# Optimization experiments

Hardware: AMD Instinct MI355X
Metric: run time of the kernel (lower is better)

## Reference

```python
import jax, jax.numpy as jnp
import numpy as np

D_MODEL = 512
N_HEADS = 8
D_HEAD = D_MODEL // N_HEADS
EPS = 1e-6


def setup_inputs() -> dict:
    key = jax.random.key(0)
    ks = jax.random.split(key, 9)
    B, S = 2, 2048
    scale = 0.02
    x = jax.random.normal(ks[0], (B, S, D_MODEL), dtype=jnp.float32)
    Wq = jax.random.normal(ks[1], (D_MODEL, D_MODEL), dtype=jnp.float32) * scale
    Wk = jax.random.normal(ks[2], (D_MODEL, D_MODEL), dtype=jnp.float32) * scale
    Wv = jax.random.normal(ks[3], (D_MODEL, D_MODEL), dtype=jnp.float32) * scale
    Wo = jax.random.normal(ks[4], (D_MODEL, D_MODEL), dtype=jnp.float32) * scale
    bq = jax.random.normal(ks[5], (D_MODEL,), dtype=jnp.float32) * scale
    bk = jax.random.normal(ks[6], (D_MODEL,), dtype=jnp.float32) * scale
    bv = jax.random.normal(ks[7], (D_MODEL,), dtype=jnp.float32) * scale
    bo = jax.random.normal(ks[8], (D_MODEL,), dtype=jnp.float32) * scale
    return {"x": x, "Wq": Wq, "bq": bq, "Wk": Wk, "bk": bk,
            "Wv": Wv, "bv": bv, "Wo": Wo, "bo": bo}


def _split_heads(t, B, S):
    # [B,S,D] -> [B,H,S,dh]
    return t.reshape(B, S, N_HEADS, D_HEAD).transpose(0, 2, 1, 3)


def reference(x, Wq, bq, Wk, bk, Wv, bv, Wo, bo):
    B, S, _ = x.shape
    q = _split_heads(x @ Wq.T + bq, B, S)
    k = _split_heads(x @ Wk.T + bk, B, S)
    v = _split_heads(x @ Wv.T + bv, B, S)
    # 'relu' kernel applied to Q and K
    q = jax.nn.relu(q)
    k = jax.nn.relu(k)
    # K_sum: [B,H,S,1] -- per-position sum over head dim; note it broadcasts
    # over the KEY axis of attn, i.e. each QUERY row n is divided by K_sum[n]
    k_sum = k.sum(axis=-1, keepdims=True)
    attn = jnp.einsum('bhnd,bhmd->bhnm', q, k) / (k_sum + EPS)
    attn = jax.nn.softmax(attn, axis=-1)
    out = jnp.einsum('bhnm,bhmd->bhnd', attn, v)
    out = out.transpose(0, 2, 1, 3).reshape(B, S, D_MODEL)
    return (out @ Wo.T + bo, attn)
```

## Files before the change

### kernel.cpp

```cpp
#include <hip/hip_runtime.h>
#include <stdint.h>


typedef __attribute__((ext_vector_type(8))) short short8;
typedef __attribute__((ext_vector_type(4))) float f4;

#define MFMA(a, b, c) __builtin_amdgcn_mfma_f32_16x16x32_bf16(a, b, c, 0, 0, 0)

struct __align__(8) us4 { uint16_t a, b, c, d; };

__device__ __forceinline__ uint16_t f2bf(float f) {
  union { float f; uint32_t u; } v; v.f = f;
  uint32_t u = v.u;
  return (uint16_t)((u + 0x7fffu + ((u >> 16) & 1u)) >> 16);
}
__device__ __forceinline__ float bf2f(uint16_t u) {
  union { uint32_t u; float f; } v; v.u = ((uint32_t)u) << 16; return v.f;
}
__device__ __forceinline__ us4 pack4(float4 v) {
  us4 r; r.a = f2bf(v.x); r.b = f2bf(v.y); r.c = f2bf(v.z); r.d = f2bf(v.w); return r;
}

__device__ __forceinline__ void async16(const uint16_t* g, uint16_t* l) {
  __builtin_amdgcn_global_load_lds(
      (const __attribute__((address_space(1))) void*)g,
      (__attribute__((address_space(3))) void*)l, 16, 0, 0);
}

__global__ __launch_bounds__(256) void convert_kernel(
    const float* __restrict__ x, const float* __restrict__ Wq,
    const float* __restrict__ Wk, const float* __restrict__ Wv,
    const float* __restrict__ Wo, uint16_t* __restrict__ xb,
    uint16_t* __restrict__ W3, uint16_t* __restrict__ Wob) {
  int i = blockIdx.x * 256 + threadIdx.x;
  ((us4*)xb)[i] = pack4(((const float4*)x)[i]);
  if (i < 65536) {
    ((us4*)W3)[i]          = pack4(((const float4*)Wq)[i]);
    ((us4*)W3)[65536 + i]  = pack4(((const float4*)Wk)[i]);
    ((us4*)W3)[131072 + i] = pack4(((const float4*)Wv)[i]);
    ((us4*)Wob)[i]         = pack4(((const float4*)Wo)[i]);
  }
}

__device__ __forceinline__ void gemm_loop(
    const uint16_t* __restrict__ A, const uint16_t* __restrict__ Bt,
    int row0, int col0, uint16_t* Alds, uint16_t* Blds, f4 (&acc)[4][4]) {
  const int tid = threadIdx.x;
  const int w = tid >> 6, lane = tid & 63;
  const int c = lane & 15, quad = lane >> 4;
  const int wm = w >> 1, wn = w & 1;
  const int srow = lane >> 2;
  const int sslot = ((lane & 3) ^ ((lane >> 2) & 3) ^ ((lane >> 4) & 3)) * 8;
  const uint16_t* Asrc = A + (size_t)(row0 + srow) * 512 + sslot;
  const uint16_t* Bsrc = Bt + (size_t)(col0 + srow) * 512 + sslot;
  const int posv = (quad ^ (c & 3) ^ (c >> 2)) * 8;
  for (int k0 = 0; k0 < 512; k0 += 32) {
    __syncthreads();
#pragma unroll
    for (int chh = 0; chh < 2; ++chh) {
      int ch = w * 2 + chh;
      async16(Asrc + (size_t)ch * 16 * 512 + k0, Alds + ch * 512);
      async16(Bsrc + (size_t)ch * 16 * 512 + k0, Blds + ch * 512);
    }
    __syncthreads();
    short8 af[4], bf[4];
#pragma unroll
    for (int mi = 0; mi < 4; ++mi)
      af[mi] = *(const short8*)&Alds[(wm * 64 + mi * 16 + c) * 32 + posv];
#pragma unroll
    for (int ni = 0; ni < 4; ++ni)
      bf[ni] = *(const short8*)&Blds[(wn * 64 + ni * 16 + c) * 32 + posv];
#pragma unroll
    for (int mi = 0; mi < 4; ++mi)
#pragma unroll
      for (int ni = 0; ni < 4; ++ni)
        acc[mi][ni] = MFMA(af[mi], bf[ni], acc[mi][ni]);
  }
}

__global__ __launch_bounds__(256) void qkv_gemm(
    const uint16_t* __restrict__ xb, const uint16_t* __restrict__ W3,
    const float* __restrict__ bq, const float* __restrict__ bk,
    const float* __restrict__ bv, uint16_t* __restrict__ Qb,
    uint16_t* __restrict__ Kb, uint16_t* __restrict__ Vt) {
  __shared__ __align__(16) uint16_t Alds[128 * 32];
  __shared__ __align__(16) uint16_t Blds[128 * 32];
  __shared__ __align__(16) uint16_t Ct[128 * 136];
  f4 acc[4][4] = {};
  const int row0 = blockIdx.y * 128, col0 = blockIdx.x * 128;
  gemm_loop(xb, W3, row0, col0, Alds, Blds, acc);
  const int tid = threadIdx.x, w = tid >> 6, lane = tid & 63;
  const int c = lane & 15, quad = lane >> 4;
  const int wm = w >> 1, wn = w & 1;
  const int r3 = col0 >> 9;
  if (r3 < 2) {
    const float* bias = (r3 == 0) ? bq : bk;
    uint16_t* dst = (r3 == 0) ? Qb : Kb;
#pragma unroll
    for (int mi = 0; mi < 4; ++mi)
#pragma unroll
      for (int ni = 0; ni < 4; ++ni)
#pragma unroll
        for (int r = 0; r < 4; ++r) {
          int row = row0 + wm * 64 + mi * 16 + quad * 4 + r;
          int col = col0 + wn * 64 + ni * 16 + c;
          int o = col & 511;
          float v = acc[mi][ni][r] + bias[o];
          dst[(size_t)row * 512 + o] = f2bf(fmaxf(v, 0.0f));
        }
  } else {
#pragma unroll
    for (int mi = 0; mi < 4; ++mi)
#pragma unroll
      for (int ni = 0; ni < 4; ++ni)
#pragma unroll
        for (int r = 0; r < 4; ++r) {
          int sl = wm * 64 + mi * 16 + quad * 4 + r;
          int cl = wn * 64 + ni * 16 + c;
          int o = (col0 + cl) & 511;
          Ct[sl * 136 + cl] = f2bf(acc[mi][ni][r] + bv[o]);
        }
    __syncthreads();
    const int b = row0 >> 11, s0 = row0 & 2047;
    const int cl = tid >> 1, half = tid & 1;
    const int ocol = (col0 - 1024) + cl;
    uint16_t* vdst = Vt + (size_t)(b * 512 + ocol) * 2048 + s0 + half * 64;
#pragma unroll
    for (int g = 0; g < 8; ++g) {
      union { short8 v; uint16_t e[8]; } o8;
#pragma unroll
      for (int jj = 0; jj < 8; ++jj)
        o8.e[jj] = Ct[(half * 64 + g * 8 + jj) * 136 + cl];
      *(short8*)(vdst + g * 8) = o8.v;
    }
  }
}

__global__ __launch_bounds__(256) void proj_gemm(
    const uint16_t* __restrict__ Ob, const uint16_t* __restrict__ Wob,
    const float* __restrict__ bo, float* __restrict__ out) {
  __shared__ __align__(16) uint16_t Alds[128 * 32];
  __shared__ __align__(16) uint16_t Blds[128 * 32];
  f4 acc[4][4] = {};
  const int row0 = blockIdx.y * 128, col0 = blockIdx.x * 128;
  gemm_loop(Ob, Wob, row0, col0, Alds, Blds, acc);
  const int tid = threadIdx.x, w = tid >> 6, lane = tid & 63;
  const int c = lane & 15, quad = lane >> 4;
  const int wm = w >> 1, wn = w & 1;
#pragma unroll
  for (int mi = 0; mi < 4; ++mi)
#pragma unroll
    for (int ni = 0; ni < 4; ++ni)
#pragma unroll
      for (int r = 0; r < 4; ++r) {
        int row = row0 + wm * 64 + mi * 16 + quad * 4 + r;
        int col = col0 + wn * 64 + ni * 16 + c;
        out[(size_t)row * 512 + col] = acc[mi][ni][r] + bo[col];
      }
}

__global__ __launch_bounds__(256) void ksum_kernel(
    const uint16_t* __restrict__ Kb, float* __restrict__ rq) {
  int t = blockIdx.x * 256 + threadIdx.x;
  int row = t >> 2, part = t & 3;
  const uint4* p = (const uint4*)(Kb + (size_t)row * 64 + part * 16);
  float s = 0.f;
#pragma unroll
  for (int g = 0; g < 2; ++g) {
    union { uint4 u; uint16_t e[8]; } v; v.u = p[g];
#pragma unroll
    for (int j = 0; j < 8; ++j) s += bf2f(v.e[j]);
  }
  s += __shfl_xor(s, 1, 4);
  s += __shfl_xor(s, 2, 4);
  if (part == 0) rq[row] = 1.0f / (s + 1e-6f);
}

__global__ __launch_bounds__(256) void attn_kernel(
    const uint16_t* __restrict__ Qb, const uint16_t* __restrict__ Kb,
    const uint16_t* __restrict__ Vt, const float* __restrict__ rq,
    float* __restrict__ attn, uint16_t* __restrict__ Ob) {
  __shared__ __align__(16) uint16_t Klds[64 * 64];
  __shared__ __align__(16) uint16_t Vlds[64 * 64];
  __shared__ __align__(16) float Pw[4][16 * 64];
  const int tid = threadIdx.x, w = tid >> 6, lane = tid & 63;
  const int c = lane & 15, quad = lane >> 4, c7 = c & 7;
  const int bid = blockIdx.x;
  const int bh = (bid & 7) * 2 + ((bid >> 3) & 1);
  const int qt = bid >> 4;
  const int b = bh >> 3, h = bh & 7;
  const int n0 = qt * 64;
  const int rbase = b * 2048 + n0;
  const uint16_t* qptr = Qb + (size_t)(rbase + w * 16 + c) * 512 + h * 64 + quad * 8;
  short8 aq0 = *(const short8*)qptr;
  short8 aq1 = *(const short8*)(qptr + 32);
  float rqv[4];
#pragma unroll
  for (int r = 0; r < 4; ++r)
    rqv[r] = rq[(size_t)(rbase + w * 16 + quad * 4 + r) * 8 + h];
  const int vsrow = lane >> 3;
  const int vslot = ((lane & 7) ^ vsrow) * 8;
  const uint16_t* Ksrc = Kb + (size_t)(b * 2048) * 512 + h * 64 + vslot;
  const uint16_t* Vsrc = Vt + (size_t)(bh * 64) * 2048 + vslot;

  float lsum[4] = {0.f, 0.f, 0.f, 0.f};
  for (int kt = 0; kt < 32; ++kt) {
    __syncthreads();
#pragma unroll
    for (int chh = 0; chh < 2; ++chh) {
      int ch = w * 2 + chh;
      async16(Ksrc + (size_t)(kt * 64 + ch * 8 + vsrow) * 512, Klds + ch * 512);
    }
    __syncthreads();
#pragma unroll
    for (int ni = 0; ni < 4; ++ni) {
      const uint16_t* kp = &Klds[(ni * 16 + c) * 64];
      short8 bk0 = *(const short8*)(kp + ((quad ^ c7) * 8));
      short8 bk1 = *(const short8*)(kp + (((quad + 4) ^ c7) * 8));
      f4 s = {};
      s = MFMA(aq0, bk0, s);
      s = MFMA(aq1, bk1, s);
#pragma unroll
      for (int r = 0; r < 4; ++r) lsum[r] += __expf(s[r] * rqv[r]);
    }
  }
  float rli[4];
#pragma unroll
  for (int r = 0; r < 4; ++r) {
    float v = lsum[r];
    v += __shfl_xor(v, 1, 16);
    v += __shfl_xor(v, 2, 16);
    v += __shfl_xor(v, 4, 16);
    v += __shfl_xor(v, 8, 16);
    rli[r] = 1.0f / v;
  }

  f4 oacc[4] = {};
  float* arowc = attn + ((size_t)bh * 2048 + n0 + w * 16 + c) * 2048;
  float* Pme = Pw[w];
  for (int kt = 0; kt < 32; ++kt) {
    __syncthreads();
#pragma unroll
    for (int chh = 0; chh < 2; ++chh) {
      int ch = w * 2 + chh;
      async16(Ksrc + (size_t)(kt * 64 + ch * 8 + vsrow) * 512, Klds + ch * 512);
      async16(Vsrc + (size_t)(ch * 8 + vsrow) * 2048 + kt * 64, Vlds + ch * 512);
    }
    __syncthreads();
#pragma unroll
    for (int ni = 0; ni < 4; ++ni) {
      const uint16_t* kp = &Klds[(ni * 16 + c) * 64];
      short8 bk0 = *(const short8*)(kp + ((quad ^ c7) * 8));
      short8 bk1 = *(const short8*)(kp + (((quad + 4) ^ c7) * 8));
      f4 s = {};
      s = MFMA(aq0, bk0, s);
      s = MFMA(aq1, bk1, s);
#pragma unroll
      for (int r = 0; r < 4; ++r) {
        int rowp = quad * 4 + r;
        float p = __expf(s[r] * rqv[r]) * rli[r];
        Pme[rowp * 64 + (((ni * 4 + (c >> 2)) ^ rowp) * 4) + (c & 3)] = p;
      }
    }
    asm volatile("s_waitcnt lgkmcnt(0)" ::: "memory");
#pragma unroll
    for (int ks = 0; ks < 2; ++ks) {
      int ch0 = ks * 8 + quad * 2;
      f4 p0 = *(const f4*)&Pme[c * 64 + ((ch0 ^ c) * 4)];
      f4 p1 = *(const f4*)&Pme[c * 64 + (((ch0 + 1) ^ c) * 4)];
      *(f4*)&arowc[kt * 64 + ch0 * 4] = p0;
      *(f4*)&arowc[kt * 64 + ch0 * 4 + 4] = p1;
      union { short8 v; uint16_t e[8]; } ap;
#pragma unroll
      for (int i = 0; i < 4; ++i) { ap.e[i] = f2bf(p0[i]); ap.e[4 + i] = f2bf(p1[i]); }
#pragma unroll
      for (int nj = 0; nj < 4; ++nj) {
        short8 bvv = *(const short8*)&Vlds[(nj * 16 + c) * 64 +
                                           (((ks * 4 + quad) ^ c7) * 8)];
        oacc[nj] = MFMA(ap.v, bvv, oacc[nj]);
      }
    }
  }
#pragma unroll
  for (int nj = 0; nj < 4; ++nj)
#pragma unroll
    for (int r = 0; r < 4; ++r)
      Ob[(size_t)(rbase + w * 16 + quad * 4 + r) * 512 + h * 64 + nj * 16 + c] =
          f2bf(oacc[nj][r]);
}

extern "C" void kernel_launch(void* const* d_in, const int* in_sizes, int n_in,
                              void* d_out, int out_size, void* d_ws, size_t ws_size,
                              hipStream_t stream) {
  const float* x  = (const float*)d_in[0];
  const float* Wq = (const float*)d_in[1];
  const float* bq = (const float*)d_in[2];
  const float* Wk = (const float*)d_in[3];
  const float* bk = (const float*)d_in[4];
  const float* Wv = (const float*)d_in[5];
  const float* bv = (const float*)d_in[6];
  const float* Wo = (const float*)d_in[7];
  const float* bo = (const float*)d_in[8];

  float* out0 = (float*)d_out;
  float* attn = out0 + (size_t)2 * 2048 * 512;

  uint8_t* ws = (uint8_t*)d_ws;
  uint16_t* xb  = (uint16_t*)(ws);
  uint16_t* W3  = (uint16_t*)(ws + 0x400000);
  uint16_t* Wob = (uint16_t*)(ws + 0x580000);
  uint16_t* Qb  = (uint16_t*)(ws + 0x600000);
  uint16_t* Kb  = (uint16_t*)(ws + 0xA00000);
  uint16_t* Vt  = (uint16_t*)(ws + 0xE00000);
  uint16_t* Ob  = (uint16_t*)(ws + 0x1200000);
  float*    rq  = (float*)  (ws + 0x1600000);

  convert_kernel<<<2048, 256, 0, stream>>>(x, Wq, Wk, Wv, Wo, xb, W3, Wob);
  qkv_gemm<<<dim3(12, 32), 256, 0, stream>>>(xb, W3, bq, bk, bv, Qb, Kb, Vt);
  ksum_kernel<<<512, 256, 0, stream>>>(Kb, rq);
  attn_kernel<<<512, 256, 0, stream>>>(Qb, Kb, Vt, rq, attn, Ob);
  proj_gemm<<<dim3(4, 32), 256, 0, stream>>>(Ob, Wob, bo, out0);
}
```

Measured before the change: 382.8 us.

## Double-buffer LDS tiles in GEMM and attention loops to overlap loads

Adds ping-pong LDS buffers to the shared GEMM loop and to both attention passes. The next K/V or A/B tile is issued with async global-to-LDS loads before computing on the current tile, and each iteration needs only one barrier instead of two. The aim is to hide global-load latency behind MFMA and exp work. In exchange it uses more LDS, which can lower occupancy. It also relies on the one end-of-iteration barrier being enough to ensure the async loads have completed, since no explicit vmcnt wait is added.

Result: no change. 378.6 us (-1.1%).

```diff
diff --git a/kernel.cpp b/kernel.cpp
--- a/kernel.cpp
+++ b/kernel.cpp
@@ -44,7 +44,8 @@
 
 __device__ __forceinline__ void gemm_loop(
     const uint16_t* __restrict__ A, const uint16_t* __restrict__ Bt,
-    int row0, int col0, uint16_t* Alds, uint16_t* Blds, f4 (&acc)[4][4]) {
+    int row0, int col0, uint16_t* A0, uint16_t* B0,
+    uint16_t* A1, uint16_t* B1, f4 (&acc)[4][4]) {
   const int tid = threadIdx.x;
   const int w = tid >> 6, lane = tid & 63;
   const int c = lane & 15, quad = lane >> 4;
@@ -54,27 +55,39 @@
   const uint16_t* Asrc = A + (size_t)(row0 + srow) * 512 + sslot;
   const uint16_t* Bsrc = Bt + (size_t)(col0 + srow) * 512 + sslot;
   const int posv = (quad ^ (c & 3) ^ (c >> 2)) * 8;
+#pragma unroll
+  for (int chh = 0; chh < 2; ++chh) {
+    int ch = w * 2 + chh;
+    async16(Asrc + (size_t)ch * 16 * 512, A0 + ch * 512);
+    async16(Bsrc + (size_t)ch * 16 * 512, B0 + ch * 512);
+  }
+  __syncthreads();
   for (int k0 = 0; k0 < 512; k0 += 32) {
+    const uint16_t* Ac = (k0 & 32) ? A1 : A0;
+    const uint16_t* Bc = (k0 & 32) ? B1 : B0;
+    if (k0 + 32 < 512) {
+      uint16_t* An = (k0 & 32) ? A0 : A1;
+      uint16_t* Bn = (k0 & 32) ? B0 : B1;
+#pragma unroll
+      for (int chh = 0; chh < 2; ++chh) {
+        int ch = w * 2 + chh;
+        async16(Asrc + (size_t)ch * 16 * 512 + (k0 + 32), An + ch * 512);
+        async16(Bsrc + (size_t)ch * 16 * 512 + (k0 + 32), Bn + ch * 512);
+      }
+    }
+    short8 af[4], bfr[4];
+#pragma unroll
+    for (int mi = 0; mi < 4; ++mi)
+      af[mi] = *(const short8*)&Ac[(wm * 64 + mi * 16 + c) * 32 + posv];
+#pragma unroll
+    for (int ni = 0; ni < 4; ++ni)
+      bfr[ni] = *(const short8*)&Bc[(wn * 64 + ni * 16 + c) * 32 + posv];
+#pragma unroll
+    for (int mi = 0; mi < 4; ++mi)
+#pragma unroll
+      for (int ni = 0; ni < 4; ++ni)
+        acc[mi][ni] = MFMA(af[mi], bfr[ni], acc[mi][ni]);
     __syncthreads();
-#pragma unroll
-    for (int chh = 0; chh < 2; ++chh) {
-      int ch = w * 2 + chh;
-      async16(Asrc + (size_t)ch * 16 * 512 + k0, Alds + ch * 512);
-      async16(Bsrc + (size_t)ch * 16 * 512 + k0, Blds + ch * 512);
-    }
-    __syncthreads();
-    short8 af[4], bf[4];
-#pragma unroll
-    for (int mi = 0; mi < 4; ++mi)
-      af[mi] = *(const short8*)&Alds[(wm * 64 + mi * 16 + c) * 32 + posv];
-#pragma unroll
-    for (int ni = 0; ni < 4; ++ni)
-      bf[ni] = *(const short8*)&Blds[(wn * 64 + ni * 16 + c) * 32 + posv];
-#pragma unroll
-    for (int mi = 0; mi < 4; ++mi)
-#pragma unroll
-      for (int ni = 0; ni < 4; ++ni)
-        acc[mi][ni] = MFMA(af[mi], bf[ni], acc[mi][ni]);
   }
 }
 
@@ -83,12 +96,15 @@
     const float* __restrict__ bq, const float* __restrict__ bk,
     const float* __restrict__ bv, uint16_t* __restrict__ Qb,
     uint16_t* __restrict__ Kb, uint16_t* __restrict__ Vt) {
-  __shared__ __align__(16) uint16_t Alds[128 * 32];
-  __shared__ __align__(16) uint16_t Blds[128 * 32];
-  __shared__ __align__(16) uint16_t Ct[128 * 136];
+  __shared__ __align__(16) uint16_t smem[25600];
+  uint16_t* A0 = smem;
+  uint16_t* B0 = smem + 4096;
+  uint16_t* A1 = smem + 8192;
+  uint16_t* B1 = smem + 12288;
+  uint16_t* Ct = smem + 8192;
   f4 acc[4][4] = {};
   const int row0 = blockIdx.y * 128, col0 = blockIdx.x * 128;
-  gemm_loop(xb, W3, row0, col0, Alds, Blds, acc);
+  gemm_loop(xb, W3, row0, col0, A0, B0, A1, B1, acc);
   const int tid = threadIdx.x, w = tid >> 6, lane = tid & 63;
   const int c = lane & 15, quad = lane >> 4;
   const int wm = w >> 1, wn = w & 1;
@@ -139,11 +155,14 @@
 __global__ __launch_bounds__(256) void proj_gemm(
     const uint16_t* __restrict__ Ob, const uint16_t* __restrict__ Wob,
     const float* __restrict__ bo, float* __restrict__ out) {
-  __shared__ __align__(16) uint16_t Alds[128 * 32];
-  __shared__ __align__(16) uint16_t Blds[128 * 32];
+  __shared__ __align__(16) uint16_t smem[16384];
+  uint16_t* A0 = smem;
+  uint16_t* B0 = smem + 4096;
+  uint16_t* A1 = smem + 8192;
+  uint16_t* B1 = smem + 12288;
   f4 acc[4][4] = {};
   const int row0 = blockIdx.y * 128, col0 = blockIdx.x * 128;
-  gemm_loop(Ob, Wob, row0, col0, Alds, Blds, acc);
+  gemm_loop(Ob, Wob, row0, col0, A0, B0, A1, B1, acc);
   const int tid = threadIdx.x, w = tid >> 6, lane = tid & 63;
   const int c = lane & 15, quad = lane >> 4;
   const int wm = w >> 1, wn = w & 1;
@@ -180,8 +199,8 @@
     const uint16_t* __restrict__ Qb, const uint16_t* __restrict__ Kb,
     const uint16_t* __restrict__ Vt, const float* __restrict__ rq,
     float* __restrict__ attn, uint16_t* __restrict__ Ob) {
-  __shared__ __align__(16) uint16_t Klds[64 * 64];
-  __shared__ __align__(16) uint16_t Vlds[64 * 64];
+  __shared__ __align__(16) uint16_t Klds[2][64 * 64];
+  __shared__ __align__(16) uint16_t Vlds[2][64 * 64];
   __shared__ __align__(16) float Pw[4][16 * 64];
   const int tid = threadIdx.x, w = tid >> 6, lane = tid & 63;
   const int c = lane & 15, quad = lane >> 4, c7 = c & 7;
@@ -204,17 +223,26 @@
   const uint16_t* Vsrc = Vt + (size_t)(bh * 64) * 2048 + vslot;
 
   float lsum[4] = {0.f, 0.f, 0.f, 0.f};
+#pragma unroll
+  for (int chh = 0; chh < 2; ++chh) {
+    int ch = w * 2 + chh;
+    async16(Ksrc + (size_t)(ch * 8 + vsrow) * 512, Klds[0] + ch * 512);
+  }
+  __syncthreads();
   for (int kt = 0; kt < 32; ++kt) {
-    __syncthreads();
-#pragma unroll
-    for (int chh = 0; chh < 2; ++chh) {
-      int ch = w * 2 + chh;
-      async16(Ksrc + (size_t)(kt * 64 + ch * 8 + vsrow) * 512, Klds + ch * 512);
-    }
-    __syncthreads();
+    const uint16_t* Kc = Klds[kt & 1];
+    if (kt < 31) {
+      uint16_t* Kn = Klds[(kt & 1) ^ 1];
+#pragma unroll
+      for (int chh = 0; chh < 2; ++chh) {
+        int ch = w * 2 + chh;
+        async16(Ksrc + (size_t)((kt + 1) * 64 + ch * 8 + vsrow) * 512,
+                Kn + ch * 512);
+      }
+    }
 #pragma unroll
     for (int ni = 0; ni < 4; ++ni) {
-      const uint16_t* kp = &Klds[(ni * 16 + c) * 64];
+      const uint16_t* kp = &Kc[(ni * 16 + c) * 64];
       short8 bk0 = *(const short8*)(kp + ((quad ^ c7) * 8));
       short8 bk1 = *(const short8*)(kp + (((quad + 4) ^ c7) * 8));
       f4 s = {};
@@ -223,6 +251,7 @@
 #pragma unroll
       for (int r = 0; r < 4; ++r) lsum[r] += __expf(s[r] * rqv[r]);
     }
+    __syncthreads();
   }
   float rli[4];
 #pragma unroll
@@ -238,18 +267,32 @@
   f4 oacc[4] = {};
   float* arowc = attn + ((size_t)bh * 2048 + n0 + w * 16 + c) * 2048;
   float* Pme = Pw[w];
+#pragma unroll
+  for (int chh = 0; chh < 2; ++chh) {
+    int ch = w * 2 + chh;
+    async16(Ksrc + (size_t)(ch * 8 + vsrow) * 512, Klds[0] + ch * 512);
+    async16(Vsrc + (size_t)(ch * 8 + vsrow) * 2048, Vlds[0] + ch * 512);
+  }
+  __syncthreads();
   for (int kt = 0; kt < 32; ++kt) {
-    __syncthreads();
-#pragma unroll
-    for (int chh = 0; chh < 2; ++chh) {
-      int ch = w * 2 + chh;
-      async16(Ksrc + (size_t)(kt * 64 + ch * 8 + vsrow) * 512, Klds + ch * 512);
-      async16(Vsrc + (size_t)(ch * 8 + vsrow) * 2048 + kt * 64, Vlds + ch * 512);
-    }
-    __syncthreads();
+    const int cur = kt & 1;
+    const uint16_t* Kc = Klds[cur];
+    const uint16_t* Vc = Vlds[cur];
+    if (kt < 31) {
+      uint16_t* Kn = Klds[cur ^ 1];
+      uint16_t* Vn = Vlds[cur ^ 1];
+#pragma unroll
+      for (int chh = 0; chh < 2; ++chh) {
+        int ch = w * 2 + chh;
+        async16(Ksrc + (size_t)((kt + 1) * 64 + ch * 8 + vsrow) * 512,
+                Kn + ch * 512);
+        async16(Vsrc + (size_t)(ch * 8 + vsrow) * 2048 + (kt + 1) * 64,
+                Vn + ch * 512);
+      }
+    }
 #pragma unroll
     for (int ni = 0; ni < 4; ++ni) {
-      const uint16_t* kp = &Klds[(ni * 16 + c) * 64];
+      const uint16_t* kp = &Kc[(ni * 16 + c) * 64];
       short8 bk0 = *(const short8*)(kp + ((quad ^ c7) * 8));
       short8 bk1 = *(const short8*)(kp + (((quad + 4) ^ c7) * 8));
       f4 s = {};
@@ -275,11 +318,12 @@
       for (int i = 0; i < 4; ++i) { ap.e[i] = f2bf(p0[i]); ap.e[4 + i] = f2bf(p1[i]); }
 #pragma unroll
       for (int nj = 0; nj < 4; ++nj) {
-        short8 bvv = *(const short8*)&Vlds[(nj * 16 + c) * 64 +
-                                           (((ks * 4 + quad) ^ c7) * 8)];
+        short8 bvv = *(const short8*)&Vc[(nj * 16 + c) * 64 +
+                                         (((ks * 4 + quad) ^ c7) * 8)];
         oacc[nj] = MFMA(ap.v, bvv, oacc[nj]);
       }
     }
+    __syncthreads();
   }
 #pragma unroll
   for (int nj = 0; nj < 4; ++nj)
```
